# Performance work log

Hardware: AMD Instinct MI355X
Metric: run time of the kernel (lower is better)

The kernel has to match this reference:

```python
import jax, jax.numpy as jnp
import numpy as np

E, N_NODES, D, OUT, FDIM = 1_000_000, 50_000, 16, 64, 256


def setup_inputs() -> dict:
    key = jax.random.key(0)
    ks = jax.random.split(key, 16)
    s = 0.1  # param scale (stand-in for xavier init)
    return {
        "Sij": jax.random.uniform(ks[0], (E,), jnp.float32),
        "Cijj": jax.random.normal(ks[1], (E, D, D), jnp.float32),
        "dst": jax.random.randint(ks[2], (E,), 0, N_NODES, dtype=jnp.int32),
        "N": N_NODES,
        "Wc": jax.random.normal(ks[3], (OUT, D), jnp.float32) * s,
        "alphaC": jax.random.normal(ks[4], (D, 1), jnp.float32) * s,
        "alphaf": jax.random.normal(ks[5], (FDIM, 1), jnp.float32) * s,
        "b": jax.random.normal(ks[6], (OUT, 1), jnp.float32) * s,
        "w": jax.random.normal(ks[7], (1, OUT), jnp.float32) * s,
        "Wf": jax.random.normal(ks[8], (OUT, FDIM), jnp.float32) * s,
        "bias": jax.random.normal(ks[9], (OUT, 1), jnp.float32) * s,
        "W1": jax.random.normal(ks[10], (FDIM, D), jnp.float32) * s,
        "b1": jax.random.normal(ks[11], (FDIM,), jnp.float32) * s,
        "W2": jax.random.normal(ks[12], (1, D), jnp.float32) * s,
        "b2": jax.random.normal(ks[13], (1,), jnp.float32) * s,
    }


def reference(Sij, Cijj, dst, N, Wc, alphaC, alphaf, b, w, Wf, bias, W1, b1, W2, b2):
    # apply_edges: per-edge scalar * correlation matrix  -> [E, D, D]
    tmp = Sij[:, None, None] * Cijj
    # update_all: mailbox sum over incoming edges -> per-node correlation [N, D, D]
    corr = jax.ops.segment_sum(tmp, dst, num_segments=N)
    # attention logit per node: w @ (Wc @ corr_i @ alphaC + Wf @ alphaf + b)
    v = corr @ alphaC                                  # [N, D, 1]
    wc_v = jnp.einsum('od,ndk->nok', Wc, v)            # [N, OUT, 1]
    c0 = Wf @ alphaf + b                               # [OUT, 1] (node-independent)
    logits = jnp.einsum('po,nok->n', w, wc_v + c0)     # [N]
    att = jax.nn.softmax(logits)                       # softmax over all nodes
    # Ci = sum_n att_n * corr_n  -> [D, D]
    Ci = jnp.einsum('n,nij->ij', att, corr)
    # small MLP tail
    Fi = jax.nn.sigmoid(jax.nn.relu(Ci @ W1.T + b1))   # [D, FDIM]
    Fi2 = jax.nn.relu(Fi.T @ W2.T + b2)                # [FDIM, 1]
    P = (Wf @ Fi2 + bias).T                            # [1, OUT]
    return P
```

## Files before the change

### kernel.cpp

```cpp
#include <hip/hip_runtime.h>
#include <hip/hip_bf16.h>


#define NNODES 50000
#define CAP 96

typedef float f32x4 __attribute__((ext_vector_type(4)));

__device__ __forceinline__ unsigned f2o(float f) {
    unsigned u = __float_as_uint(f);
    return (u & 0x80000000u) ? ~u : (u | 0x80000000u);
}
__device__ __forceinline__ float o2f(unsigned u) {
    return (u & 0x80000000u) ? __uint_as_float(u ^ 0x80000000u)
                             : __uint_as_float(~u);
}

__global__ void k_max(const float* __restrict__ logits,
                      unsigned* __restrict__ mEnc, int N) {
    __shared__ float red[4];
    int t = blockIdx.x * blockDim.x + threadIdx.x;
    int stride = gridDim.x * blockDim.x;
    float mx = -1e30f;
    for (int i = t; i < N; i += stride) mx = fmaxf(mx, logits[i]);
    #pragma unroll
    for (int off = 32; off; off >>= 1) mx = fmaxf(mx, __shfl_down(mx, off, 64));
    int lt = threadIdx.x;
    if ((lt & 63) == 0) red[lt >> 6] = mx;
    __syncthreads();
    if (lt == 0) {
        float m = red[0];
        for (int i = 1; i < (int)(blockDim.x >> 6); ++i) m = fmaxf(m, red[i]);
        atomicMax(mEnc, f2o(m));
    }
}

__global__ void k_exp(const float* __restrict__ logits,
                      const unsigned* __restrict__ mEnc,
                      float* __restrict__ att,
                      float* __restrict__ Z, int N) {
    __shared__ float red[4];
    float m = o2f(*mEnc);
    int t = blockIdx.x * blockDim.x + threadIdx.x;
    int stride = gridDim.x * blockDim.x;
    float s = 0.f;
    for (int i = t; i < N; i += stride) {
        float e = __expf(logits[i] - m);
        att[i] = e;
        s += e;
    }
    #pragma unroll
    for (int off = 32; off; off >>= 1) s += __shfl_down(s, off, 64);
    int lt = threadIdx.x;
    if ((lt & 63) == 0) red[lt >> 6] = s;
    __syncthreads();
    if (lt == 0) {
        float ss = 0.f;
        for (int i = 0; i < (int)(blockDim.x >> 6); ++i) ss += red[i];
        atomicAdd(Z, ss);
    }
}

__global__ void k_tail(const float* __restrict__ Ci,
                       const float* __restrict__ Z,
                       const float* __restrict__ W1,
                       const float* __restrict__ b1,
                       const float* __restrict__ W2,
                       const float* __restrict__ b2,
                       const float* __restrict__ Wf,
                       const float* __restrict__ bias,
                       float* __restrict__ out) {
    __shared__ float ci[256];
    __shared__ float fi2[256];
    int t = threadIdx.x;
    float invZ = 1.f / Z[0];
    ci[t] = Ci[t] * invZ;
    __syncthreads();

    float w1row[16];
    #pragma unroll
    for (int j = 0; j < 16; ++j) w1row[j] = W1[t * 16 + j];
    float bb = b1[t];
    float g = 0.f;
    #pragma unroll
    for (int i = 0; i < 16; ++i) {
        float s = bb;
        #pragma unroll
        for (int j = 0; j < 16; ++j) s = fmaf(ci[i * 16 + j], w1row[j], s);
        s = fmaxf(s, 0.f);
        float sg = 1.f / (1.f + __expf(-s));
        g = fmaf(sg, W2[i], g);
    }
    fi2[t] = fmaxf(g + b2[0], 0.f);
    __syncthreads();

    if (t < 64) {
        float s = bias[t];
        for (int f = 0; f < 256; ++f) s = fmaf(Wf[t * 256 + f], fi2[f], s);
        out[t] = s;
    }
}

__global__ void k_init(const float* __restrict__ Wc,
                       const float* __restrict__ alphaC,
                       const float* __restrict__ w,
                       float* __restrict__ M,
                       int* __restrict__ counts,
                       float* __restrict__ Ci,
                       float* __restrict__ Z,
                       unsigned* __restrict__ mEnc,
                       int N) {
    int t = blockIdx.x * blockDim.x + threadIdx.x;
    int stride = gridDim.x * blockDim.x;
    for (int i = t; i < N; i += stride) counts[i] = 0;
    if (blockIdx.x == 0) {
        __shared__ float wWc[16];
        int tt = threadIdx.x;
        if (tt < 16) {
            float s = 0.f;
            for (int o = 0; o < 64; ++o) s = fmaf(w[o], Wc[o * 16 + tt], s);
            wWc[tt] = s;
        }
        __syncthreads();
        M[tt]  = wWc[tt >> 4] * alphaC[tt & 15];
        Ci[tt] = 0.f;
        if (tt == 0) { Z[0] = 0.f; mEnc[0] = 0u; }
    }
}

__global__ void k_build(const int* __restrict__ dst,
                        int* __restrict__ counts,
                        int* __restrict__ eidx,
                        int E) {
    int t = blockIdx.x * blockDim.x + threadIdx.x;
    int stride = gridDim.x * blockDim.x;
    for (int e = t; e < E; e += stride) {
        int d = dst[e];
        int pos = atomicAdd(&counts[d], 1);
        if (pos < CAP) eidx[d * CAP + pos] = e;
    }
}

__global__ void k_nodes(const float* __restrict__ Sij,
                        const float* __restrict__ C,
                        const int* __restrict__ counts,
                        const int* __restrict__ eidx,
                        const float* __restrict__ M,
                        float* __restrict__ corr,
                        float* __restrict__ logits) {
    int n = blockIdx.x;
    int t = threadIdx.x;
    int cnt = counts[n];
    if (cnt > CAP) cnt = CAP;

    __shared__ int   se[CAP];
    __shared__ float sw[CAP];
    if (t < cnt) {
        int e = eidx[n * CAP + t];
        se[t] = e;
        sw[t] = Sij[e];
    }
    __syncthreads();

    float a0 = 0.f, a1 = 0.f, a2 = 0.f, a3 = 0.f;
    int i = 0;
    for (; i + 4 <= cnt; i += 4) {
        size_t b0 = ((size_t)se[i])     << 8;
        size_t b1 = ((size_t)se[i + 1]) << 8;
        size_t b2 = ((size_t)se[i + 2]) << 8;
        size_t b3 = ((size_t)se[i + 3]) << 8;
        float c0 = __builtin_nontemporal_load(C + b0 + t);
        float c1 = __builtin_nontemporal_load(C + b1 + t);
        float c2 = __builtin_nontemporal_load(C + b2 + t);
        float c3 = __builtin_nontemporal_load(C + b3 + t);
        a0 = fmaf(sw[i],     c0, a0);
        a1 = fmaf(sw[i + 1], c1, a1);
        a2 = fmaf(sw[i + 2], c2, a2);
        a3 = fmaf(sw[i + 3], c3, a3);
    }
    for (; i < cnt; ++i) {
        float c = __builtin_nontemporal_load(C + (((size_t)se[i]) << 8) + t);
        a0 = fmaf(sw[i], c, a0);
    }
    float acc = (a0 + a1) + (a2 + a3);
    corr[(size_t)n * 256 + t] = acc;

    float s = acc * M[t];
    #pragma unroll
    for (int off = 32; off; off >>= 1) s += __shfl_down(s, off, 64);
    __shared__ float red[4];
    if ((t & 63) == 0) red[t >> 6] = s;
    __syncthreads();
    if (t == 0) logits[n] = red[0] + red[1] + red[2] + red[3];
}

__global__ void k_ci2(const float* __restrict__ corr,
                      const float* __restrict__ att,
                      float* __restrict__ Ci, int N) {
    int t = threadIdx.x;
    int chunk = (N + gridDim.x - 1) / gridDim.x;
    int n0 = blockIdx.x * chunk;
    int n1 = n0 + chunk; if (n1 > N) n1 = N;
    float a0 = 0.f, a1 = 0.f;
    int n = n0;
    for (; n + 2 <= n1; n += 2) {
        a0 = fmaf(att[n],     corr[(size_t)n * 256 + t],       a0);
        a1 = fmaf(att[n + 1], corr[(size_t)(n + 1) * 256 + t], a1);
    }
    if (n < n1) a0 = fmaf(att[n], corr[(size_t)n * 256 + t], a0);
    atomicAdd(&Ci[t], a0 + a1);
}

__global__ void k_init_fb(const float* __restrict__ Wc,
                          const float* __restrict__ alphaC,
                          const float* __restrict__ w,
                          float* __restrict__ M,
                          float* __restrict__ logits,
                          float* __restrict__ Ci,
                          float* __restrict__ Z,
                          unsigned* __restrict__ mEnc,
                          int N) {
    int t = blockIdx.x * blockDim.x + threadIdx.x;
    int stride = gridDim.x * blockDim.x;
    for (int i = t; i < N; i += stride) logits[i] = 0.f;
    if (blockIdx.x == 0) {
        __shared__ float wWc[16];
        int tt = threadIdx.x;
        if (tt < 16) {
            float s = 0.f;
            for (int o = 0; o < 64; ++o) s = fmaf(w[o], Wc[o * 16 + tt], s);
            wWc[tt] = s;
        }
        __syncthreads();
        M[tt]  = wWc[tt >> 4] * alphaC[tt & 15];
        Ci[tt] = 0.f;
        if (tt == 0) { Z[0] = 0.f; mEnc[0] = 0u; }
    }
}

__global__ void k_logits_stream(const float* __restrict__ Sij,
                                const f32x4* __restrict__ C,
                                const int* __restrict__ dst,
                                const float* __restrict__ M,
                                float* __restrict__ logits,
                                int E) {
    int t = blockIdx.x * blockDim.x + threadIdx.x;
    int lane = t & 63;
    int sub  = lane >> 4;
    int eoff = lane & 15;
    int gwid  = t >> 6;
    int waves = (gridDim.x * blockDim.x) >> 6;

    const f32x4* M4 = reinterpret_cast<const f32x4*>(M);
    f32x4 m0 = M4[eoff], m1 = M4[16 + eoff], m2 = M4[32 + eoff], m3 = M4[48 + eoff];

    int nq = (E + 3) >> 2;
    for (int q = gwid; q < nq; q += waves) {
        int e = (q << 2) + sub;
        float d = 0.f;
        if (e < E) {
            size_t base = (size_t)e * 64 + eoff;
            f32x4 c0 = C[base];
            f32x4 c1 = C[base + 16];
            f32x4 c2 = C[base + 32];
            f32x4 c3 = C[base + 48];
            d = c0[0]*m0[0] + c0[1]*m0[1] + c0[2]*m0[2] + c0[3]*m0[3];
            d = fmaf(c1[0], m1[0], fmaf(c1[1], m1[1], fmaf(c1[2], m1[2], fmaf(c1[3], m1[3], d))));
            d = fmaf(c2[0], m2[0], fmaf(c2[1], m2[1], fmaf(c2[2], m2[2], fmaf(c2[3], m2[3], d))));
            d = fmaf(c3[0], m3[0], fmaf(c3[1], m3[1], fmaf(c3[2], m3[2], fmaf(c3[3], m3[3], d))));
        }
        #pragma unroll
        for (int off = 8; off; off >>= 1) d += __shfl_down(d, off, 16);
        if (eoff == 0 && e < E) atomicAdd(&logits[dst[e]], Sij[e] * d);
    }
}

__global__ void k_ci_stream(const float* __restrict__ Sij,
                            const f32x4* __restrict__ C,
                            const int* __restrict__ dst,
                            const float* __restrict__ att,
                            float* __restrict__ Ci,
                            int E) {
    int t = threadIdx.x;
    int lane = t & 63;
    int sub  = lane >> 4;
    int eoff = lane & 15;
    int gwid  = (blockIdx.x * blockDim.x + t) >> 6;
    int waves = (gridDim.x * blockDim.x) >> 6;

    f32x4 a0 = 0.f, a1 = 0.f, a2 = 0.f, a3 = 0.f;
    int nq = (E + 3) >> 2;
    for (int q = gwid; q < nq; q += waves) {
        int qq = nq - 1 - q;
        int e = (qq << 2) + sub;
        if (e < E) {
            float wgt = att[dst[e]] * Sij[e];
            size_t base = (size_t)e * 64 + eoff;
            f32x4 c0 = __builtin_nontemporal_load(C + base);
            f32x4 c1 = __builtin_nontemporal_load(C + base + 16);
            f32x4 c2 = __builtin_nontemporal_load(C + base + 32);
            f32x4 c3 = __builtin_nontemporal_load(C + base + 48);
            a0 += wgt * c0;
            a1 += wgt * c1;
            a2 += wgt * c2;
            a3 += wgt * c3;
        }
    }
    __shared__ f32x4 part[256][4];
    part[t][0] = a0;
    part[t][1] = a1;
    part[t][2] = a2;
    part[t][3] = a3;
    __syncthreads();
    int k  = t & 3;
    int f4 = t >> 2;
    int eo = f4 & 15;
    int j  = f4 >> 4;
    float s = 0.f;
    #pragma unroll
    for (int wv = 0; wv < 4; ++wv)
        #pragma unroll
        for (int sb = 0; sb < 4; ++sb)
            s += part[wv * 64 + sb * 16 + eo][j][k];
    atomicAdd(&Ci[t], s);
}

extern "C" void kernel_launch(void* const* d_in, const int* in_sizes, int n_in,
                              void* d_out, int out_size, void* d_ws, size_t ws_size,
                              hipStream_t stream) {
    const float* Sij    = (const float*)d_in[0];
    const float* Cijj   = (const float*)d_in[1];
    const int*   dst    = (const int*)d_in[2];
    const float* Wc     = (const float*)d_in[4];
    const float* alphaC = (const float*)d_in[5];
    const float* w_     = (const float*)d_in[8];
    const float* Wf     = (const float*)d_in[9];
    const float* bias   = (const float*)d_in[10];
    const float* W1     = (const float*)d_in[11];
    const float* b1     = (const float*)d_in[12];
    const float* W2     = (const float*)d_in[13];
    const float* b2     = (const float*)d_in[14];

    const int E = in_sizes[0];
    const int N = NNODES;

    size_t need = (size_t)N * 4 + (size_t)N * CAP * 4 + (size_t)N * 256 * 4
                + (size_t)N * 4 * 2 + (256 + 256 + 2) * 4 + 64;

    if (ws_size >= need) {
        int*   counts = (int*)d_ws;
        int*   eidx   = counts + N;
        float* corr   = (float*)(eidx + (size_t)N * CAP);
        float* logits = corr + (size_t)N * 256;
        float* att    = logits + N;
        float* M      = att + N;
        float* Ci     = M + 256;
        float* Z      = Ci + 256;
        unsigned* mEnc = (unsigned*)(Z + 1);

        k_init <<<64, 256, 0, stream>>>(Wc, alphaC, w_, M, counts, Ci, Z, mEnc, N);
        k_build<<<2048, 256, 0, stream>>>(dst, counts, eidx, E);
        k_nodes<<<N, 256, 0, stream>>>(Sij, Cijj, counts, eidx, M, corr, logits);
        k_max  <<<50, 256, 0, stream>>>(logits, mEnc, N);
        k_exp  <<<50, 256, 0, stream>>>(logits, mEnc, att, Z, N);
        k_ci2  <<<256, 256, 0, stream>>>(corr, att, Ci, N);
        k_tail <<<1, 256, 0, stream>>>(Ci, Z, W1, b1, W2, b2, Wf, bias, (float*)d_out);
    } else {
        float* logits = (float*)d_ws;
        float* att    = logits + N;
        float* M      = att + N;
        float* Ci     = M + 256;
        float* Z      = Ci + 256;
        unsigned* mEnc = (unsigned*)(Z + 1);

        k_init_fb<<<64, 256, 0, stream>>>(Wc, alphaC, w_, M, logits, Ci, Z, mEnc, N);
        k_logits_stream<<<2048, 256, 0, stream>>>(Sij, (const f32x4*)Cijj, dst, M, logits, E);
        k_max<<<50, 256, 0, stream>>>(logits, mEnc, N);
        k_exp<<<50, 256, 0, stream>>>(logits, mEnc, att, Z, N);
        k_ci_stream<<<2048, 256, 0, stream>>>(Sij, (const f32x4*)Cijj, dst, att, Ci, E);
        k_tail<<<1, 256, 0, stream>>>(Ci, Z, W1, b1, W2, b2, Wf, bias, (float*)d_out);
    }
}
```

Measured before the change: 348.7 us.

## Vectorize per-node gather across waves and fuse exp into weighted sum

k_nodes now gives each of its four waves a different subset of the incoming edges and has it load whole 1 KB edge matrices as float4. The per-wave partial sums are then combined through shared memory, which gives wider, more coalesced loads and more loads in flight. The separate exp/normalizer kernel is folded into the weighted corr sum (k_wsum), removing one launch and the att buffer round trip. The costs are an extra LDS reduction and barrier in k_nodes, and the exp now runs per chunk inside the reduction kernel.

```diff
diff --git a/kernel.cpp b/kernel.cpp
--- a/kernel.cpp
+++ b/kernel.cpp
@@ -32,32 +32,6 @@
         float m = red[0];
         for (int i = 1; i < (int)(blockDim.x >> 6); ++i) m = fmaxf(m, red[i]);
         atomicMax(mEnc, f2o(m));
-    }
-}
-
-__global__ void k_exp(const float* __restrict__ logits,
-                      const unsigned* __restrict__ mEnc,
-                      float* __restrict__ att,
-                      float* __restrict__ Z, int N) {
-    __shared__ float red[4];
-    float m = o2f(*mEnc);
-    int t = blockIdx.x * blockDim.x + threadIdx.x;
-    int stride = gridDim.x * blockDim.x;
-    float s = 0.f;
-    for (int i = t; i < N; i += stride) {
-        float e = __expf(logits[i] - m);
-        att[i] = e;
-        s += e;
-    }
-    #pragma unroll
-    for (int off = 32; off; off >>= 1) s += __shfl_down(s, off, 64);
-    int lt = threadIdx.x;
-    if ((lt & 63) == 0) red[lt >> 6] = s;
-    __syncthreads();
-    if (lt == 0) {
-        float ss = 0.f;
-        for (int i = 0; i < (int)(blockDim.x >> 6); ++i) ss += red[i];
-        atomicAdd(Z, ss);
     }
 }
 
@@ -142,7 +116,7 @@
 }
 
 __global__ void k_nodes(const float* __restrict__ Sij,
-                        const float* __restrict__ C,
+                        const f32x4* __restrict__ C4,
                         const int* __restrict__ counts,
                         const int* __restrict__ eidx,
                         const float* __restrict__ M,
@@ -150,6 +124,8 @@
                         float* __restrict__ logits) {
     int n = blockIdx.x;
     int t = threadIdx.x;
+    int w = t >> 6;
+    int l = t & 63;
     int cnt = counts[n];
     if (cnt > CAP) cnt = CAP;
 
@@ -162,53 +138,78 @@
     }
     __syncthreads();
 
-    float a0 = 0.f, a1 = 0.f, a2 = 0.f, a3 = 0.f;
-    int i = 0;
-    for (; i + 4 <= cnt; i += 4) {
-        size_t b0 = ((size_t)se[i])     << 8;
-        size_t b1 = ((size_t)se[i + 1]) << 8;
-        size_t b2 = ((size_t)se[i + 2]) << 8;
-        size_t b3 = ((size_t)se[i + 3]) << 8;
-        float c0 = __builtin_nontemporal_load(C + b0 + t);
-        float c1 = __builtin_nontemporal_load(C + b1 + t);
-        float c2 = __builtin_nontemporal_load(C + b2 + t);
-        float c3 = __builtin_nontemporal_load(C + b3 + t);
-        a0 = fmaf(sw[i],     c0, a0);
-        a1 = fmaf(sw[i + 1], c1, a1);
-        a2 = fmaf(sw[i + 2], c2, a2);
-        a3 = fmaf(sw[i + 3], c3, a3);
-    }
-    for (; i < cnt; ++i) {
-        float c = __builtin_nontemporal_load(C + (((size_t)se[i]) << 8) + t);
-        a0 = fmaf(sw[i], c, a0);
-    }
-    float acc = (a0 + a1) + (a2 + a3);
-    corr[(size_t)n * 256 + t] = acc;
-
-    float s = acc * M[t];
-    #pragma unroll
-    for (int off = 32; off; off >>= 1) s += __shfl_down(s, off, 64);
+    f32x4 a0 = 0.f, a1 = 0.f;
+    int i = w;
+    for (; i + 4 < cnt; i += 8) {
+        size_t bA = ((size_t)se[i])     << 6;
+        size_t bB = ((size_t)se[i + 4]) << 6;
+        f32x4 cA = __builtin_nontemporal_load(C4 + bA + l);
+        f32x4 cB = __builtin_nontemporal_load(C4 + bB + l);
+        a0 += sw[i]     * cA;
+        a1 += sw[i + 4] * cB;
+    }
+    if (i < cnt) {
+        f32x4 c = __builtin_nontemporal_load(C4 + (((size_t)se[i]) << 6) + l);
+        a0 += sw[i] * c;
+    }
+    f32x4 acc = a0 + a1;
+
+    __shared__ f32x4 part[4][64];
+    part[w][l] = acc;
+    __syncthreads();
+    int ll = t >> 2, kk = t & 3;
+    float s = part[0][ll][kk] + part[1][ll][kk] + part[2][ll][kk] + part[3][ll][kk];
+    corr[(size_t)n * 256 + t] = s;
+
+    float d = s * M[t];
+    #pragma unroll
+    for (int off = 32; off; off >>= 1) d += __shfl_down(d, off, 64);
     __shared__ float red[4];
-    if ((t & 63) == 0) red[t >> 6] = s;
+    if ((t & 63) == 0) red[t >> 6] = d;
     __syncthreads();
     if (t == 0) logits[n] = red[0] + red[1] + red[2] + red[3];
 }
 
-__global__ void k_ci2(const float* __restrict__ corr,
-                      const float* __restrict__ att,
-                      float* __restrict__ Ci, int N) {
+__global__ void k_wsum(const float* __restrict__ logits,
+                       const unsigned* __restrict__ mEnc,
+                       const float* __restrict__ corr,
+                       float* __restrict__ Z,
+                       float* __restrict__ Ci, int N) {
+    __shared__ float satt[256];
+    __shared__ float red[4];
+    float m = o2f(*mEnc);
     int t = threadIdx.x;
     int chunk = (N + gridDim.x - 1) / gridDim.x;
     int n0 = blockIdx.x * chunk;
     int n1 = n0 + chunk; if (n1 > N) n1 = N;
-    float a0 = 0.f, a1 = 0.f;
-    int n = n0;
-    for (; n + 2 <= n1; n += 2) {
-        a0 = fmaf(att[n],     corr[(size_t)n * 256 + t],       a0);
-        a1 = fmaf(att[n + 1], corr[(size_t)(n + 1) * 256 + t], a1);
-    }
-    if (n < n1) a0 = fmaf(att[n], corr[(size_t)n * 256 + t], a0);
-    atomicAdd(&Ci[t], a0 + a1);
+
+    float zpart = 0.f;
+    float a = 0.f;
+    for (int base = n0; base < n1; base += 256) {
+        int nn = n1 - base; if (nn > 256) nn = 256;
+        float e = 0.f;
+        if (t < nn) e = __expf(logits[base + t] - m);
+        satt[t] = e;
+        zpart += e;
+        __syncthreads();
+        int j = 0;
+        for (; j + 4 <= nn; j += 4) {
+            a = fmaf(satt[j],     corr[(size_t)(base + j)     * 256 + t], a);
+            a = fmaf(satt[j + 1], corr[(size_t)(base + j + 1) * 256 + t], a);
+            a = fmaf(satt[j + 2], corr[(size_t)(base + j + 2) * 256 + t], a);
+            a = fmaf(satt[j + 3], corr[(size_t)(base + j + 3) * 256 + t], a);
+        }
+        for (; j < nn; ++j)
+            a = fmaf(satt[j], corr[(size_t)(base + j) * 256 + t], a);
+        __syncthreads();
+    }
+    atomicAdd(&Ci[t], a);
+
+    #pragma unroll
+    for (int off = 32; off; off >>= 1) zpart += __shfl_down(zpart, off, 64);
+    if ((t & 63) == 0) red[t >> 6] = zpart;
+    __syncthreads();
+    if (t == 0) atomicAdd(Z, red[0] + red[1] + red[2] + red[3]);
 }
 
 __global__ void k_init_fb(const float* __restrict__ Wc,
@@ -235,6 +236,32 @@
         M[tt]  = wWc[tt >> 4] * alphaC[tt & 15];
         Ci[tt] = 0.f;
         if (tt == 0) { Z[0] = 0.f; mEnc[0] = 0u; }
+    }
+}
+
+__global__ void k_exp_fb(const float* __restrict__ logits,
+                         const unsigned* __restrict__ mEnc,
+                         float* __restrict__ att,
+                         float* __restrict__ Z, int N) {
+    __shared__ float red[4];
+    float m = o2f(*mEnc);
+    int t = blockIdx.x * blockDim.x + threadIdx.x;
+    int stride = gridDim.x * blockDim.x;
+    float s = 0.f;
+    for (int i = t; i < N; i += stride) {
+        float e = __expf(logits[i] - m);
+        att[i] = e;
+        s += e;
+    }
+    #pragma unroll
+    for (int off = 32; off; off >>= 1) s += __shfl_down(s, off, 64);
+    int lt = threadIdx.x;
+    if ((lt & 63) == 0) red[lt >> 6] = s;
+    __syncthreads();
+    if (lt == 0) {
+        float ss = 0.f;
+        for (int i = 0; i < (int)(blockDim.x >> 6); ++i) ss += red[i];
+        atomicAdd(Z, ss);
     }
 }
 
@@ -345,25 +372,24 @@
     const int N = NNODES;
 
     size_t need = (size_t)N * 4 + (size_t)N * CAP * 4 + (size_t)N * 256 * 4
-                + (size_t)N * 4 * 2 + (256 + 256 + 2) * 4 + 64;
+                + (size_t)N * 4 + (256 + 256 + 2) * 4 + 64;
 
     if (ws_size >= need) {
         int*   counts = (int*)d_ws;
         int*   eidx   = counts + N;
         float* corr   = (float*)(eidx + (size_t)N * CAP);
         float* logits = corr + (size_t)N * 256;
-        float* att    = logits + N;
-        float* M      = att + N;
+        float* M      = logits + N;
         float* Ci     = M + 256;
         float* Z      = Ci + 256;
         unsigned* mEnc = (unsigned*)(Z + 1);
 
         k_init <<<64, 256, 0, stream>>>(Wc, alphaC, w_, M, counts, Ci, Z, mEnc, N);
         k_build<<<2048, 256, 0, stream>>>(dst, counts, eidx, E);
-        k_nodes<<<N, 256, 0, stream>>>(Sij, Cijj, counts, eidx, M, corr, logits);
+        k_nodes<<<N, 256, 0, stream>>>(Sij, (const f32x4*)Cijj, counts, eidx, M,
+                                       corr, logits);
         k_max  <<<50, 256, 0, stream>>>(logits, mEnc, N);
-        k_exp  <<<50, 256, 0, stream>>>(logits, mEnc, att, Z, N);
-        k_ci2  <<<256, 256, 0, stream>>>(corr, att, Ci, N);
+        k_wsum <<<256, 256, 0, stream>>>(logits, mEnc, corr, Z, Ci, N);
         k_tail <<<1, 256, 0, stream>>>(Ci, Z, W1, b1, W2, b2, Wf, bias, (float*)d_out);
     } else {
         float* logits = (float*)d_ws;
@@ -376,7 +402,7 @@
         k_init_fb<<<64, 256, 0, stream>>>(Wc, alphaC, w_, M, logits, Ci, Z, mEnc, N);
         k_logits_stream<<<2048, 256, 0, stream>>>(Sij, (const f32x4*)Cijj, dst, M, logits, E);
         k_max<<<50, 256, 0, stream>>>(logits, mEnc, N);
-        k_exp<<<50, 256, 0, stream>>>(logits, mEnc, att, Z, N);
+        k_exp_fb<<<50, 256, 0, stream>>>(logits, mEnc, att, Z, N);
         k_ci_stream<<<2048, 256, 0, stream>>>(Sij, (const f32x4*)Cijj, dst, att, Ci, E);
         k_tail<<<1, 256, 0, stream>>>(Ci, Z, W1, b1, W2, b2, Wf, bias, (float*)d_out);
     }
```

Result: faster. 321.1 us (-7.9%).
